# Optimization experiments

Measured on AMD Instinct MI355X. Metric: run time of the kernel, lower is better.

Reference implementation:

```python
import jax, jax.numpy as jnp
import numpy as np

EPS = 1e-8


def setup_inputs() -> dict:
    key = jax.random.key(0)
    k1, k2, k3 = jax.random.split(key, 3)
    n_nodes, n_pos, d, n_seg = 50000, 2048, 128, 32
    pred = jax.random.normal(k1, (n_nodes, d), dtype=jnp.float32)
    target = jax.random.normal(k2, (n_pos, d), dtype=jnp.float32)
    target_identifiers = jax.random.randint(k3, (n_pos,), 0, n_seg, dtype=jnp.int64)
    return {
        "pred": pred,
        "target": target,
        "target_identifiers": target_identifiers,
        "num_segments": n_seg,
    }


def reference(pred, target, target_identifiers, num_segments):
    # Pairwise L2 distance: sqrt(||t||^2 - 2 t.p + ||p||^2 + eps)
    # avoids materializing the [n_pos, n_nodes, d] broadcast tensor.
    t2 = jnp.sum(target * target, axis=-1, keepdims=True)          # [n_pos, 1]
    p2 = jnp.sum(pred * pred, axis=-1)                             # [n_nodes]
    cross = jnp.einsum('pd,nd->pn', target, pred)                  # [n_pos, n_nodes]
    sq = jnp.maximum(t2 - 2.0 * cross + p2[None, :], 0.0)
    dist_mat = jnp.sqrt(sq + EPS)                                  # [n_pos, n_nodes]

    # stage1: scatter_mean over target_identifiers (dim=0)
    seg_sum = jax.ops.segment_sum(dist_mat, target_identifiers,
                                  num_segments=num_segments)       # [n_seg, n_nodes]
    counts = jax.ops.segment_sum(jnp.ones((dist_mat.shape[0],), dist_mat.dtype),
                                 target_identifiers, num_segments=num_segments)
    seg_mean = seg_sum / jnp.maximum(counts, 1.0)[:, None]

    # stage2: mean over segments
    return seg_mean.mean(axis=0)                                   # [n_nodes]
```

## Files before the change

### kernel.cpp

```cpp
#include <hip/hip_runtime.h>

#define DIMK 128

typedef __bf16 bf16x8 __attribute__((ext_vector_type(8)));
typedef float  f32x4  __attribute__((ext_vector_type(4)));

__device__ inline unsigned short f32_to_bf16_rne(float f) {
    unsigned u = __float_as_uint(f);
    u += 0x7FFFu + ((u >> 16) & 1u);
    return (unsigned short)(u >> 16);
}


__global__ void pack_rows(const float* __restrict__ src,
                          unsigned short* __restrict__ dst,
                          float* __restrict__ norm2,
                          int n_valid, int n_rows_pad, float scale) {
    int wave = threadIdx.x >> 6, lane = threadIdx.x & 63;
    int row = blockIdx.x * 4 + wave;
    if (row >= n_rows_pad) return;
    int srow = min(row, n_valid - 1);
    int e = lane * 2;
    float2 v = *(const float2*)(src + (size_t)srow * DIMK + e);
    unsigned pk = (unsigned)f32_to_bf16_rne(scale * v.x) |
                  ((unsigned)f32_to_bf16_rne(scale * v.y) << 16);
    int tile = row >> 4, col = row & 15;
    int kk = e >> 5, kb = (e >> 3) & 3, j = e & 7;
    size_t off = (size_t)tile * 2048 + kk * 512 + (kb * 16 + col) * 8 + j;
    *(unsigned*)(dst + off) = pk;
    float s = v.x * v.x + v.y * v.y;
#pragma unroll
    for (int o = 1; o < 64; o <<= 1) s += __shfl_xor(s, o, 64);
    if (lane == 0) norm2[row] = s;
}

__global__ void seg_weights(const int* __restrict__ ids,
                            const int* __restrict__ nseg_p,
                            const float* __restrict__ t2,
                            float2* __restrict__ tw, int n_pos) {
    __shared__ int   cnt[256];
    __shared__ float w[256];
    int nseg = nseg_p[0];
    if (nseg > 256) nseg = 256;
    int t = threadIdx.x;
    if (t < nseg) cnt[t] = 0;
    __syncthreads();
    for (int p = t; p < n_pos; p += blockDim.x) atomicAdd(&cnt[ids[p]], 1);
    __syncthreads();
    if (t < nseg) w[t] = 1.0f / ((float)nseg * (float)max(cnt[t], 1));
    __syncthreads();
    for (int p = t; p < n_pos; p += blockDim.x) {
        float2 e; e.x = t2[p]; e.y = w[ids[p]];
        tw[p] = e;
    }
}

#define SLICE_TILES 8
__global__ __launch_bounds__(256, 4)
void l2dist_main(const unsigned short* __restrict__ pb,
                 const float* __restrict__ p2,
                 const unsigned short* __restrict__ tb,
                 const float2* __restrict__ tw,
                 float* __restrict__ out,
                 int n_nodes) {
    __shared__ __align__(16) unsigned short lbuf[SLICE_TILES][2048];
    __shared__ __align__(16) float tw_lds[SLICE_TILES * 32];

    const int tid  = threadIdx.x;
    const int lane = tid & 63;
    const int wave = tid >> 6;
    const int col  = lane & 15;
    const int kb   = lane >> 4;
    const int n0   = blockIdx.x * 128 + wave * 32;

    bf16x8 bfrag[2][4];
    float p2g[2];
    const unsigned short* bp = pb + ((size_t)(n0 >> 4)) * 2048 + (size_t)lane * 8;
#pragma unroll
    for (int g = 0; g < 2; ++g) {
#pragma unroll
        for (int kk = 0; kk < 4; ++kk)
            bfrag[g][kk] = *(const bf16x8*)(bp + g * 2048 + kk * 512);
        p2g[g] = p2[n0 + g * 16 + col];
    }

    const int pbase = blockIdx.y * SLICE_TILES;

    if (tid < SLICE_TILES * 16) {
        float2 e = tw[pbase * 16 + tid];
        tw_lds[2 * tid]     = e.x;
        tw_lds[2 * tid + 1] = e.y;
    }

    const unsigned short* sgp = tb + (size_t)pbase * 2048 + wave * 512 + lane * 8;
    unsigned short* ldst = &lbuf[0][0] + wave * 512;
#pragma unroll
    for (int t = 0; t < SLICE_TILES; ++t) {
        __builtin_amdgcn_global_load_lds(
            (const __attribute__((address_space(1))) unsigned int*)(const void*)
                (sgp + (size_t)t * 2048),
            (__attribute__((address_space(3))) unsigned int*)(void*)
                (ldst + t * 2048),
            16, 0, 0);
    }
    __syncthreads();

    float acc0 = 0.f, acc1 = 0.f;
#pragma unroll
    for (int t = 0; t < SLICE_TILES; ++t) {
        const unsigned short* rb = &lbuf[t][lane * 8];
        bf16x8 a0 = *(const bf16x8*)(rb);
        bf16x8 a1 = *(const bf16x8*)(rb + 512);
        bf16x8 a2 = *(const bf16x8*)(rb + 1024);
        bf16x8 a3 = *(const bf16x8*)(rb + 1536);

        f32x4 d0 = {0.f, 0.f, 0.f, 0.f};
        f32x4 d1 = {0.f, 0.f, 0.f, 0.f};
        d0 = __builtin_amdgcn_mfma_f32_16x16x32_bf16(a0, bfrag[0][0], d0, 0, 0, 0);
        d1 = __builtin_amdgcn_mfma_f32_16x16x32_bf16(a0, bfrag[1][0], d1, 0, 0, 0);
        d0 = __builtin_amdgcn_mfma_f32_16x16x32_bf16(a1, bfrag[0][1], d0, 0, 0, 0);
        d1 = __builtin_amdgcn_mfma_f32_16x16x32_bf16(a1, bfrag[1][1], d1, 0, 0, 0);
        d0 = __builtin_amdgcn_mfma_f32_16x16x32_bf16(a2, bfrag[0][2], d0, 0, 0, 0);
        d1 = __builtin_amdgcn_mfma_f32_16x16x32_bf16(a2, bfrag[1][2], d1, 0, 0, 0);
        d0 = __builtin_amdgcn_mfma_f32_16x16x32_bf16(a3, bfrag[0][3], d0, 0, 0, 0);
        d1 = __builtin_amdgcn_mfma_f32_16x16x32_bf16(a3, bfrag[1][3], d1, 0, 0, 0);

        f32x4 w0 = *(const f32x4*)&tw_lds[(t * 16 + kb * 4) * 2];
        f32x4 w1 = *(const f32x4*)&tw_lds[(t * 16 + kb * 4) * 2 + 4];
        float t2v[4] = {w0[0], w0[2], w1[0], w1[2]};
        float wv[4]  = {w0[1], w0[3], w1[1], w1[3]};
#pragma unroll
        for (int j = 0; j < 4; ++j) {
            float s0 = d0[j] + (t2v[j] + p2g[0]);
            float s1 = d1[j] + (t2v[j] + p2g[1]);
            acc0 = fmaf(wv[j], __builtin_amdgcn_sqrtf(fmaxf(s0, 0.f)), acc0);
            acc1 = fmaf(wv[j], __builtin_amdgcn_sqrtf(fmaxf(s1, 0.f)), acc1);
        }
    }

    acc0 += __shfl_xor(acc0, 16, 64);
    acc0 += __shfl_xor(acc0, 32, 64);
    acc1 += __shfl_xor(acc1, 16, 64);
    acc1 += __shfl_xor(acc1, 32, 64);
    if (lane < 16) {
        int na = n0 + col;
        int nb = n0 + 16 + col;
        if (na < n_nodes) atomicAdd(out + na, acc0);
        if (nb < n_nodes) atomicAdd(out + nb, acc1);
    }
}

extern "C" void kernel_launch(void* const* d_in, const int* in_sizes, int n_in,
                              void* d_out, int out_size, void* d_ws, size_t ws_size,
                              hipStream_t stream) {
    const float* pred  = (const float*)d_in[0];
    const float* tgt   = (const float*)d_in[1];
    const int*   ids   = (const int*)d_in[2];
    const int*   nsegp = (const int*)d_in[3];
    float* out = (float*)d_out;

    int n_nodes = in_sizes[0] / DIMK;
    int n_pos   = in_sizes[2];

    int gx = (n_nodes + 127) / 128;
    int n_rows_pad = gx * 128;

    char* ws = (char*)d_ws;
    size_t off_pb = 0;
    size_t off_tb = off_pb + (size_t)n_rows_pad * DIMK * 2;
    size_t off_p2 = off_tb + (size_t)n_pos * DIMK * 2;
    size_t off_t2 = off_p2 + (size_t)n_rows_pad * 4;
    size_t off_tw = off_t2 + (size_t)n_pos * 4;
    unsigned short* pb = (unsigned short*)(ws + off_pb);
    unsigned short* tb = (unsigned short*)(ws + off_tb);
    float*          p2 = (float*)(ws + off_p2);
    float*          t2 = (float*)(ws + off_t2);
    float2*         tw = (float2*)(ws + off_tw);

    pack_rows<<<(n_rows_pad + 3) / 4, 256, 0, stream>>>(pred, pb, p2, n_nodes, n_rows_pad, 1.0f);
    pack_rows<<<(n_pos + 3) / 4, 256, 0, stream>>>(tgt, tb, t2, n_pos, n_pos, -2.0f);
    seg_weights<<<1, 1024, 0, stream>>>(ids, nsegp, t2, tw, n_pos);
    hipMemsetAsync(out, 0, (size_t)out_size * sizeof(float), stream);

    int ys = (n_pos >> 4) / SLICE_TILES;
    dim3 grid(gx, ys);
    l2dist_main<<<grid, 256, 0, stream>>>(pb, p2, tb, tw, out, n_nodes);
}
```

Measured before the change: 58.94 us.

## Halve target slice per block, swap grid axes, prefetch weights from global

Cuts the target tiles each block processes from 8 to 4, doubling the grid and the number of atomic adds to the output. The grid axes are swapped so that consecutive blocks share the same pred rows and walk through different target slices. The per-row t2 and weight values are now read straight from global memory into registers with a one-tile-ahead prefetch, replacing the LDS staging. Launch bounds rise to 6 blocks per CU. This aims to raise occupancy and improve L2 locality for the pred fragments, at the cost of reloading pred fragments twice as often and doubling atomic traffic.

Result: slower. 62.29 us (+5.7%).

```diff
diff --git a/kernel.cpp b/kernel.cpp
--- a/kernel.cpp
+++ b/kernel.cpp
@@ -1,6 +1,7 @@
 #include <hip/hip_runtime.h>
 
 #define DIMK 128
+#define SLICE_TILES 4
 
 typedef __bf16 bf16x8 __attribute__((ext_vector_type(8)));
 typedef float  f32x4  __attribute__((ext_vector_type(4)));
@@ -55,8 +56,7 @@
     }
 }
 
-#define SLICE_TILES 8
-__global__ __launch_bounds__(256, 4)
+__global__ __launch_bounds__(256, 6)
 void l2dist_main(const unsigned short* __restrict__ pb,
                  const float* __restrict__ p2,
                  const unsigned short* __restrict__ tb,
@@ -64,14 +64,25 @@
                  float* __restrict__ out,
                  int n_nodes) {
     __shared__ __align__(16) unsigned short lbuf[SLICE_TILES][2048];
-    __shared__ __align__(16) float tw_lds[SLICE_TILES * 32];
-
     const int tid  = threadIdx.x;
     const int lane = tid & 63;
     const int wave = tid >> 6;
     const int col  = lane & 15;
     const int kb   = lane >> 4;
-    const int n0   = blockIdx.x * 128 + wave * 32;
+    const int n0   = blockIdx.y * 128 + wave * 32;
+
+    const int pbase = blockIdx.x * SLICE_TILES;
+    const unsigned short* sgp = tb + (size_t)pbase * 2048 + wave * 512 + lane * 8;
+    unsigned short* ldst = &lbuf[0][0] + wave * 512;
+#pragma unroll
+    for (int t = 0; t < SLICE_TILES; ++t) {
+        __builtin_amdgcn_global_load_lds(
+            (const __attribute__((address_space(1))) unsigned int*)(const void*)
+                (sgp + (size_t)t * 2048),
+            (__attribute__((address_space(3))) unsigned int*)(void*)
+                (ldst + t * 2048),
+            16, 0, 0);
+    }
 
     bf16x8 bfrag[2][4];
     float p2g[2];
@@ -84,30 +95,21 @@
         p2g[g] = p2[n0 + g * 16 + col];
     }
 
-    const int pbase = blockIdx.y * SLICE_TILES;
+    const float2* twp = tw + ((size_t)pbase << 4) + kb * 4;
+    f32x4 cw0 = *(const f32x4*)(twp);
+    f32x4 cw1 = *(const f32x4*)(twp + 2);
 
-    if (tid < SLICE_TILES * 16) {
-        float2 e = tw[pbase * 16 + tid];
-        tw_lds[2 * tid]     = e.x;
-        tw_lds[2 * tid + 1] = e.y;
-    }
-
-    const unsigned short* sgp = tb + (size_t)pbase * 2048 + wave * 512 + lane * 8;
-    unsigned short* ldst = &lbuf[0][0] + wave * 512;
-#pragma unroll
-    for (int t = 0; t < SLICE_TILES; ++t) {
-        __builtin_amdgcn_global_load_lds(
-            (const __attribute__((address_space(1))) unsigned int*)(const void*)
-                (sgp + (size_t)t * 2048),
-            (__attribute__((address_space(3))) unsigned int*)(void*)
-                (ldst + t * 2048),
-            16, 0, 0);
-    }
     __syncthreads();
 
     float acc0 = 0.f, acc1 = 0.f;
 #pragma unroll
     for (int t = 0; t < SLICE_TILES; ++t) {
+        f32x4 nw0 = cw0, nw1 = cw1;
+        if (t + 1 < SLICE_TILES) {
+            nw0 = *(const f32x4*)(twp + 16 * (t + 1));
+            nw1 = *(const f32x4*)(twp + 16 * (t + 1) + 2);
+        }
+
         const unsigned short* rb = &lbuf[t][lane * 8];
         bf16x8 a0 = *(const bf16x8*)(rb);
         bf16x8 a1 = *(const bf16x8*)(rb + 512);
@@ -125,10 +127,8 @@
         d0 = __builtin_amdgcn_mfma_f32_16x16x32_bf16(a3, bfrag[0][3], d0, 0, 0, 0);
         d1 = __builtin_amdgcn_mfma_f32_16x16x32_bf16(a3, bfrag[1][3], d1, 0, 0, 0);
 
-        f32x4 w0 = *(const f32x4*)&tw_lds[(t * 16 + kb * 4) * 2];
-        f32x4 w1 = *(const f32x4*)&tw_lds[(t * 16 + kb * 4) * 2 + 4];
-        float t2v[4] = {w0[0], w0[2], w1[0], w1[2]};
-        float wv[4]  = {w0[1], w0[3], w1[1], w1[3]};
+        float t2v[4] = {cw0[0], cw0[2], cw1[0], cw1[2]};
+        float wv[4]  = {cw0[1], cw0[3], cw1[1], cw1[3]};
 #pragma unroll
         for (int j = 0; j < 4; ++j) {
             float s0 = d0[j] + (t2v[j] + p2g[0]);
@@ -136,6 +136,7 @@
             acc0 = fmaf(wv[j], __builtin_amdgcn_sqrtf(fmaxf(s0, 0.f)), acc0);
             acc1 = fmaf(wv[j], __builtin_amdgcn_sqrtf(fmaxf(s1, 0.f)), acc1);
         }
+        cw0 = nw0; cw1 = nw1;
     }
 
     acc0 += __shfl_xor(acc0, 16, 64);
@@ -162,8 +163,8 @@
     int n_nodes = in_sizes[0] / DIMK;
     int n_pos   = in_sizes[2];
 
-    int gx = (n_nodes + 127) / 128;
-    int n_rows_pad = gx * 128;
+    int gy = (n_nodes + 127) / 128;
+    int n_rows_pad = gy * 128;
 
     char* ws = (char*)d_ws;
     size_t off_pb = 0;
@@ -182,7 +183,7 @@
     seg_weights<<<1, 1024, 0, stream>>>(ids, nsegp, t2, tw, n_pos);
     hipMemsetAsync(out, 0, (size_t)out_size * sizeof(float), stream);
 
-    int ys = (n_pos >> 4) / SLICE_TILES;
-    dim3 grid(gx, ys);
+    int gx = (n_pos >> 4) / SLICE_TILES;
+    dim3 grid(gx, gy);
     l2dist_main<<<grid, 256, 0, stream>>>(pb, p2, tb, tw, out, n_nodes);
 }
```

## Enlarge main-kernel tile, double-buffer target loads, fold norms into MFMA accumulator

Applied to the files above, without the earlier changes.

Each wave now covers 64 nodes instead of 32, and each block processes 256 target rows instead of 128. The target tiles are streamed through a two-slot LDS ring of async global-to-LDS loads with explicit vmcnt waits and barriers, so loads overlap with compute. t2 and p2 are preloaded into the MFMA accumulator, which removes per-element adds. The grid is reordered so the target slice is the fast dimension and node tiles are the slow one, which halves the atomics per node relative to the work done. The cost is higher register pressure from 16 B fragments and 4 accumulators, and fewer blocks for load balancing.

Result: slower. 66.82 us (+13.4%).

```diff
diff --git a/kernel.cpp b/kernel.cpp
--- a/kernel.cpp
+++ b/kernel.cpp
@@ -36,8 +36,7 @@
 
 __global__ void seg_weights(const int* __restrict__ ids,
                             const int* __restrict__ nseg_p,
-                            const float* __restrict__ t2,
-                            float2* __restrict__ tw, int n_pos) {
+                            float* __restrict__ wsa, int n_pos) {
     __shared__ int   cnt[256];
     __shared__ float w[256];
     int nseg = nseg_p[0];
@@ -49,104 +48,133 @@
     __syncthreads();
     if (t < nseg) w[t] = 1.0f / ((float)nseg * (float)max(cnt[t], 1));
     __syncthreads();
-    for (int p = t; p < n_pos; p += blockDim.x) {
-        float2 e; e.x = t2[p]; e.y = w[ids[p]];
-        tw[p] = e;
-    }
-}
-
-#define SLICE_TILES 8
+    for (int p = t; p < n_pos; p += blockDim.x) wsa[p] = w[ids[p]];
+}
+
 __global__ __launch_bounds__(256, 4)
 void l2dist_main(const unsigned short* __restrict__ pb,
                  const float* __restrict__ p2,
                  const unsigned short* __restrict__ tb,
-                 const float2* __restrict__ tw,
+                 const float* __restrict__ t2g,
+                 const float* __restrict__ wg,
                  float* __restrict__ out,
                  int n_nodes) {
-    __shared__ __align__(16) unsigned short lbuf[SLICE_TILES][2048];
-    __shared__ __align__(16) float tw_lds[SLICE_TILES * 32];
+    __shared__ __align__(16) unsigned short lbuf[2][8192];
+    __shared__ __align__(16) float t2_lds[256];
+    __shared__ __align__(16) float w_lds[256];
 
     const int tid  = threadIdx.x;
     const int lane = tid & 63;
     const int wave = tid >> 6;
     const int col  = lane & 15;
     const int kb   = lane >> 4;
-    const int n0   = blockIdx.x * 128 + wave * 32;
-
-    bf16x8 bfrag[2][4];
-    float p2g[2];
+    const int n0   = blockIdx.y * 256 + wave * 64;
+    const int tbase = blockIdx.x * 16;
+    const int rbase = tbase * 16;
+
+    bf16x8 bfrag[4][4];
+    float p2g[4];
     const unsigned short* bp = pb + ((size_t)(n0 >> 4)) * 2048 + (size_t)lane * 8;
 #pragma unroll
-    for (int g = 0; g < 2; ++g) {
+    for (int g = 0; g < 4; ++g) {
 #pragma unroll
         for (int kk = 0; kk < 4; ++kk)
             bfrag[g][kk] = *(const bf16x8*)(bp + g * 2048 + kk * 512);
         p2g[g] = p2[n0 + g * 16 + col];
     }
 
-    const int pbase = blockIdx.y * SLICE_TILES;
-
-    if (tid < SLICE_TILES * 16) {
-        float2 e = tw[pbase * 16 + tid];
-        tw_lds[2 * tid]     = e.x;
-        tw_lds[2 * tid + 1] = e.y;
-    }
-
-    const unsigned short* sgp = tb + (size_t)pbase * 2048 + wave * 512 + lane * 8;
-    unsigned short* ldst = &lbuf[0][0] + wave * 512;
-#pragma unroll
-    for (int t = 0; t < SLICE_TILES; ++t) {
-        __builtin_amdgcn_global_load_lds(
-            (const __attribute__((address_space(1))) unsigned int*)(const void*)
-                (sgp + (size_t)t * 2048),
-            (__attribute__((address_space(3))) unsigned int*)(void*)
-                (ldst + t * 2048),
-            16, 0, 0);
-    }
-    __syncthreads();
-
-    float acc0 = 0.f, acc1 = 0.f;
-#pragma unroll
-    for (int t = 0; t < SLICE_TILES; ++t) {
-        const unsigned short* rb = &lbuf[t][lane * 8];
-        bf16x8 a0 = *(const bf16x8*)(rb);
-        bf16x8 a1 = *(const bf16x8*)(rb + 512);
-        bf16x8 a2 = *(const bf16x8*)(rb + 1024);
-        bf16x8 a3 = *(const bf16x8*)(rb + 1536);
-
-        f32x4 d0 = {0.f, 0.f, 0.f, 0.f};
-        f32x4 d1 = {0.f, 0.f, 0.f, 0.f};
-        d0 = __builtin_amdgcn_mfma_f32_16x16x32_bf16(a0, bfrag[0][0], d0, 0, 0, 0);
-        d1 = __builtin_amdgcn_mfma_f32_16x16x32_bf16(a0, bfrag[1][0], d1, 0, 0, 0);
-        d0 = __builtin_amdgcn_mfma_f32_16x16x32_bf16(a1, bfrag[0][1], d0, 0, 0, 0);
-        d1 = __builtin_amdgcn_mfma_f32_16x16x32_bf16(a1, bfrag[1][1], d1, 0, 0, 0);
-        d0 = __builtin_amdgcn_mfma_f32_16x16x32_bf16(a2, bfrag[0][2], d0, 0, 0, 0);
-        d1 = __builtin_amdgcn_mfma_f32_16x16x32_bf16(a2, bfrag[1][2], d1, 0, 0, 0);
-        d0 = __builtin_amdgcn_mfma_f32_16x16x32_bf16(a3, bfrag[0][3], d0, 0, 0, 0);
-        d1 = __builtin_amdgcn_mfma_f32_16x16x32_bf16(a3, bfrag[1][3], d1, 0, 0, 0);
-
-        f32x4 w0 = *(const f32x4*)&tw_lds[(t * 16 + kb * 4) * 2];
-        f32x4 w1 = *(const f32x4*)&tw_lds[(t * 16 + kb * 4) * 2 + 4];
-        float t2v[4] = {w0[0], w0[2], w1[0], w1[2]};
-        float wv[4]  = {w0[1], w0[3], w1[1], w1[3]};
-#pragma unroll
-        for (int j = 0; j < 4; ++j) {
-            float s0 = d0[j] + (t2v[j] + p2g[0]);
-            float s1 = d1[j] + (t2v[j] + p2g[1]);
-            acc0 = fmaf(wv[j], __builtin_amdgcn_sqrtf(fmaxf(s0, 0.f)), acc0);
-            acc1 = fmaf(wv[j], __builtin_amdgcn_sqrtf(fmaxf(s1, 0.f)), acc1);
+    __builtin_amdgcn_global_load_lds(
+        (const __attribute__((address_space(1))) unsigned int*)(const void*)
+            (t2g + rbase + wave * 64 + lane),
+        (__attribute__((address_space(3))) unsigned int*)(void*)
+            (&t2_lds[wave * 64]), 4, 0, 0);
+    __builtin_amdgcn_global_load_lds(
+        (const __attribute__((address_space(1))) unsigned int*)(const void*)
+            (wg + rbase + wave * 64 + lane),
+        (__attribute__((address_space(3))) unsigned int*)(void*)
+            (&w_lds[wave * 64]), 4, 0, 0);
+
+    const unsigned short* sgp = tb + (size_t)tbase * 2048 + wave * 512 + lane * 8;
+#define STAGE(C, B)                                                            \
+    _Pragma("unroll")                                                          \
+    for (int t_ = 0; t_ < 4; ++t_) {                                           \
+        __builtin_amdgcn_global_load_lds(                                      \
+            (const __attribute__((address_space(1))) unsigned int*)(const void*)\
+                (sgp + ((C) * 4 + t_) * 2048),                                 \
+            (__attribute__((address_space(3))) unsigned int*)(void*)           \
+                (&lbuf[B][t_ * 2048] + wave * 512),                            \
+            16, 0, 0);                                                         \
+    }
+
+    STAGE(0, 0);
+    STAGE(1, 1);
+
+    float acc0 = 0.f, acc1 = 0.f, acc2 = 0.f, acc3 = 0.f;
+
+#pragma unroll
+    for (int c = 0; c < 4; ++c) {
+        if (c < 3) { asm volatile("s_waitcnt vmcnt(4)" ::: "memory"); }
+        else       { asm volatile("s_waitcnt vmcnt(0)" ::: "memory"); }
+        __builtin_amdgcn_s_barrier();
+
+#pragma unroll
+        for (int t = 0; t < 4; ++t) {
+            const unsigned short* rb = &lbuf[c & 1][t * 2048] + lane * 8;
+            bf16x8 a0 = *(const bf16x8*)(rb);
+            bf16x8 a1 = *(const bf16x8*)(rb + 512);
+            bf16x8 a2 = *(const bf16x8*)(rb + 1024);
+            bf16x8 a3 = *(const bf16x8*)(rb + 1536);
+
+            f32x4 t2v = *(const f32x4*)&t2_lds[(c * 4 + t) * 16 + kb * 4];
+            f32x4 wv  = *(const f32x4*)&w_lds[(c * 4 + t) * 16 + kb * 4];
+
+            f32x4 d0 = t2v + p2g[0];
+            f32x4 d1 = t2v + p2g[1];
+            f32x4 d2 = t2v + p2g[2];
+            f32x4 d3 = t2v + p2g[3];
+            d0 = __builtin_amdgcn_mfma_f32_16x16x32_bf16(a0, bfrag[0][0], d0, 0, 0, 0);
+            d1 = __builtin_amdgcn_mfma_f32_16x16x32_bf16(a0, bfrag[1][0], d1, 0, 0, 0);
+            d2 = __builtin_amdgcn_mfma_f32_16x16x32_bf16(a0, bfrag[2][0], d2, 0, 0, 0);
+            d3 = __builtin_amdgcn_mfma_f32_16x16x32_bf16(a0, bfrag[3][0], d3, 0, 0, 0);
+            d0 = __builtin_amdgcn_mfma_f32_16x16x32_bf16(a1, bfrag[0][1], d0, 0, 0, 0);
+            d1 = __builtin_amdgcn_mfma_f32_16x16x32_bf16(a1, bfrag[1][1], d1, 0, 0, 0);
+            d2 = __builtin_amdgcn_mfma_f32_16x16x32_bf16(a1, bfrag[2][1], d2, 0, 0, 0);
+            d3 = __builtin_amdgcn_mfma_f32_16x16x32_bf16(a1, bfrag[3][1], d3, 0, 0, 0);
+            d0 = __builtin_amdgcn_mfma_f32_16x16x32_bf16(a2, bfrag[0][2], d0, 0, 0, 0);
+            d1 = __builtin_amdgcn_mfma_f32_16x16x32_bf16(a2, bfrag[1][2], d1, 0, 0, 0);
+            d2 = __builtin_amdgcn_mfma_f32_16x16x32_bf16(a2, bfrag[2][2], d2, 0, 0, 0);
+            d3 = __builtin_amdgcn_mfma_f32_16x16x32_bf16(a2, bfrag[3][2], d3, 0, 0, 0);
+            d0 = __builtin_amdgcn_mfma_f32_16x16x32_bf16(a3, bfrag[0][3], d0, 0, 0, 0);
+            d1 = __builtin_amdgcn_mfma_f32_16x16x32_bf16(a3, bfrag[1][3], d1, 0, 0, 0);
+            d2 = __builtin_amdgcn_mfma_f32_16x16x32_bf16(a3, bfrag[2][3], d2, 0, 0, 0);
+            d3 = __builtin_amdgcn_mfma_f32_16x16x32_bf16(a3, bfrag[3][3], d3, 0, 0, 0);
+
+#pragma unroll
+            for (int j = 0; j < 4; ++j) {
+                acc0 = fmaf(wv[j], __builtin_amdgcn_sqrtf(fmaxf(d0[j], 0.f)), acc0);
+                acc1 = fmaf(wv[j], __builtin_amdgcn_sqrtf(fmaxf(d1[j], 0.f)), acc1);
+                acc2 = fmaf(wv[j], __builtin_amdgcn_sqrtf(fmaxf(d2[j], 0.f)), acc2);
+                acc3 = fmaf(wv[j], __builtin_amdgcn_sqrtf(fmaxf(d3[j], 0.f)), acc3);
+            }
         }
-    }
-
-    acc0 += __shfl_xor(acc0, 16, 64);
-    acc0 += __shfl_xor(acc0, 32, 64);
-    acc1 += __shfl_xor(acc1, 16, 64);
-    acc1 += __shfl_xor(acc1, 32, 64);
+
+        if (c < 2) {
+            __builtin_amdgcn_s_barrier();
+            STAGE(c + 2, c & 1);
+        }
+    }
+#undef STAGE
+
+    acc0 += __shfl_xor(acc0, 16, 64);  acc0 += __shfl_xor(acc0, 32, 64);
+    acc1 += __shfl_xor(acc1, 16, 64);  acc1 += __shfl_xor(acc1, 32, 64);
+    acc2 += __shfl_xor(acc2, 16, 64);  acc2 += __shfl_xor(acc2, 32, 64);
+    acc3 += __shfl_xor(acc3, 16, 64);  acc3 += __shfl_xor(acc3, 32, 64);
     if (lane < 16) {
         int na = n0 + col;
-        int nb = n0 + 16 + col;
-        if (na < n_nodes) atomicAdd(out + na, acc0);
-        if (nb < n_nodes) atomicAdd(out + nb, acc1);
+        if (na      < n_nodes) atomicAdd(out + na,      acc0);
+        if (na + 16 < n_nodes) atomicAdd(out + na + 16, acc1);
+        if (na + 32 < n_nodes) atomicAdd(out + na + 32, acc2);
+        if (na + 48 < n_nodes) atomicAdd(out + na + 48, acc3);
     }
 }
 
@@ -162,27 +190,26 @@
     int n_nodes = in_sizes[0] / DIMK;
     int n_pos   = in_sizes[2];
 
-    int gx = (n_nodes + 127) / 128;
-    int n_rows_pad = gx * 128;
+    int gy = (n_nodes + 255) / 256;
+    int n_rows_pad = gy * 256;
 
     char* ws = (char*)d_ws;
     size_t off_pb = 0;
     size_t off_tb = off_pb + (size_t)n_rows_pad * DIMK * 2;
     size_t off_p2 = off_tb + (size_t)n_pos * DIMK * 2;
     size_t off_t2 = off_p2 + (size_t)n_rows_pad * 4;
-    size_t off_tw = off_t2 + (size_t)n_pos * 4;
-    unsigned short* pb = (unsigned short*)(ws + off_pb);
-    unsigned short* tb = (unsigned short*)(ws + off_tb);
-    float*          p2 = (float*)(ws + off_p2);
-    float*          t2 = (float*)(ws + off_t2);
-    float2*         tw = (float2*)(ws + off_tw);
+    size_t off_w  = off_t2 + (size_t)n_pos * 4;
+    unsigned short* pb  = (unsigned short*)(ws + off_pb);
+    unsigned short* tb  = (unsigned short*)(ws + off_tb);
+    float*          p2  = (float*)(ws + off_p2);
+    float*          t2  = (float*)(ws + off_t2);
+    float*          wsa = (float*)(ws + off_w);
 
     pack_rows<<<(n_rows_pad + 3) / 4, 256, 0, stream>>>(pred, pb, p2, n_nodes, n_rows_pad, 1.0f);
     pack_rows<<<(n_pos + 3) / 4, 256, 0, stream>>>(tgt, tb, t2, n_pos, n_pos, -2.0f);
-    seg_weights<<<1, 1024, 0, stream>>>(ids, nsegp, t2, tw, n_pos);
+    seg_weights<<<1, 1024, 0, stream>>>(ids, nsegp, wsa, n_pos);
     hipMemsetAsync(out, 0, (size_t)out_size * sizeof(float), stream);
 
-    int ys = (n_pos >> 4) / SLICE_TILES;
-    dim3 grid(gx, ys);
-    l2dist_main<<<grid, 256, 0, stream>>>(pb, p2, tb, tw, out, n_nodes);
-}
+    dim3 grid(n_pos / 256, gy);
+    l2dist_main<<<grid, 256, 0, stream>>>(pb, p2, tb, t2, wsa, out, n_nodes);
+}
```

## Swap grid axes, split MFMA chains, stagger LDS tiles, seed accumulators with norms

Applied to the files above, without the earlier changes.

The grid is transposed so blockIdx.x walks the target-position slices and blockIdx.y walks node blocks. Adjacent blocks now share the same pred tiles, which should improve L2 locality for the large packed pred array. Each tile's four dependent MFMAs are split into two independent accumulator chains to shorten the dependency latency, and the first chain is seeded with t2+p2 so the adds are folded in. Waves start on different LDS tiles to reduce bank conflicts, and t2 and the weights move into separate arrays so each can be read with one vector load. The target LDS load is issued before the pred fragment loads to overlap them.

New measurement: 56.07 us. 1.05x faster.

```diff
diff --git a/kernel.cpp b/kernel.cpp
--- a/kernel.cpp
+++ b/kernel.cpp
@@ -1,6 +1,8 @@
 #include <hip/hip_runtime.h>
 
 #define DIMK 128
+#define SLICE_TILES 8
+#define NODES_PER_BLOCK 128
 
 typedef __bf16 bf16x8 __attribute__((ext_vector_type(8)));
 typedef float  f32x4  __attribute__((ext_vector_type(4)));
@@ -36,8 +38,7 @@
 
 __global__ void seg_weights(const int* __restrict__ ids,
                             const int* __restrict__ nseg_p,
-                            const float* __restrict__ t2,
-                            float2* __restrict__ tw, int n_pos) {
+                            float* __restrict__ wsa, int n_pos) {
     __shared__ int   cnt[256];
     __shared__ float w[256];
     int nseg = nseg_p[0];
@@ -49,29 +50,45 @@
     __syncthreads();
     if (t < nseg) w[t] = 1.0f / ((float)nseg * (float)max(cnt[t], 1));
     __syncthreads();
-    for (int p = t; p < n_pos; p += blockDim.x) {
-        float2 e; e.x = t2[p]; e.y = w[ids[p]];
-        tw[p] = e;
-    }
+    for (int p = t; p < n_pos; p += blockDim.x) wsa[p] = w[ids[p]];
 }
 
-#define SLICE_TILES 8
 __global__ __launch_bounds__(256, 4)
 void l2dist_main(const unsigned short* __restrict__ pb,
                  const float* __restrict__ p2,
                  const unsigned short* __restrict__ tb,
-                 const float2* __restrict__ tw,
+                 const float* __restrict__ t2g,
+                 const float* __restrict__ wg,
                  float* __restrict__ out,
                  int n_nodes) {
     __shared__ __align__(16) unsigned short lbuf[SLICE_TILES][2048];
-    __shared__ __align__(16) float tw_lds[SLICE_TILES * 32];
+    __shared__ __align__(16) float t2_lds[SLICE_TILES * 16];
+    __shared__ __align__(16) float w_lds[SLICE_TILES * 16];
 
     const int tid  = threadIdx.x;
     const int lane = tid & 63;
     const int wave = tid >> 6;
     const int col  = lane & 15;
     const int kb   = lane >> 4;
-    const int n0   = blockIdx.x * 128 + wave * 32;
+    const int n0   = blockIdx.y * NODES_PER_BLOCK + wave * 32;
+
+    const int pbase = blockIdx.x * SLICE_TILES;
+    const unsigned short* sgp = tb + (size_t)pbase * 2048 + wave * 512 + lane * 8;
+    unsigned short* ldst = &lbuf[0][0] + wave * 512;
+#pragma unroll
+    for (int t = 0; t < SLICE_TILES; ++t) {
+        __builtin_amdgcn_global_load_lds(
+            (const __attribute__((address_space(1))) unsigned int*)(const void*)
+                (sgp + (size_t)t * 2048),
+            (__attribute__((address_space(3))) unsigned int*)(void*)
+                (ldst + t * 2048),
+            16, 0, 0);
+    }
+
+    if (tid < SLICE_TILES * 16) {
+        t2_lds[tid] = t2g[pbase * 16 + tid];
+        w_lds[tid]  = wg[pbase * 16 + tid];
+    }
 
     bf16x8 bfrag[2][4];
     float p2g[2];
@@ -84,57 +101,41 @@
         p2g[g] = p2[n0 + g * 16 + col];
     }
 
-    const int pbase = blockIdx.y * SLICE_TILES;
-
-    if (tid < SLICE_TILES * 16) {
-        float2 e = tw[pbase * 16 + tid];
-        tw_lds[2 * tid]     = e.x;
-        tw_lds[2 * tid + 1] = e.y;
-    }
-
-    const unsigned short* sgp = tb + (size_t)pbase * 2048 + wave * 512 + lane * 8;
-    unsigned short* ldst = &lbuf[0][0] + wave * 512;
-#pragma unroll
-    for (int t = 0; t < SLICE_TILES; ++t) {
-        __builtin_amdgcn_global_load_lds(
-            (const __attribute__((address_space(1))) unsigned int*)(const void*)
-                (sgp + (size_t)t * 2048),
-            (__attribute__((address_space(3))) unsigned int*)(void*)
-                (ldst + t * 2048),
-            16, 0, 0);
-    }
     __syncthreads();
 
     float acc0 = 0.f, acc1 = 0.f;
 #pragma unroll
     for (int t = 0; t < SLICE_TILES; ++t) {
-        const unsigned short* rb = &lbuf[t][lane * 8];
+        const int te = (t + 2 * wave) & (SLICE_TILES - 1);
+
+        const unsigned short* rb = &lbuf[te][lane * 8];
         bf16x8 a0 = *(const bf16x8*)(rb);
         bf16x8 a1 = *(const bf16x8*)(rb + 512);
         bf16x8 a2 = *(const bf16x8*)(rb + 1024);
         bf16x8 a3 = *(const bf16x8*)(rb + 1536);
 
-        f32x4 d0 = {0.f, 0.f, 0.f, 0.f};
-        f32x4 d1 = {0.f, 0.f, 0.f, 0.f};
-        d0 = __builtin_amdgcn_mfma_f32_16x16x32_bf16(a0, bfrag[0][0], d0, 0, 0, 0);
-        d1 = __builtin_amdgcn_mfma_f32_16x16x32_bf16(a0, bfrag[1][0], d1, 0, 0, 0);
-        d0 = __builtin_amdgcn_mfma_f32_16x16x32_bf16(a1, bfrag[0][1], d0, 0, 0, 0);
-        d1 = __builtin_amdgcn_mfma_f32_16x16x32_bf16(a1, bfrag[1][1], d1, 0, 0, 0);
-        d0 = __builtin_amdgcn_mfma_f32_16x16x32_bf16(a2, bfrag[0][2], d0, 0, 0, 0);
-        d1 = __builtin_amdgcn_mfma_f32_16x16x32_bf16(a2, bfrag[1][2], d1, 0, 0, 0);
-        d0 = __builtin_amdgcn_mfma_f32_16x16x32_bf16(a3, bfrag[0][3], d0, 0, 0, 0);
-        d1 = __builtin_amdgcn_mfma_f32_16x16x32_bf16(a3, bfrag[1][3], d1, 0, 0, 0);
+        f32x4 t2v = *(const f32x4*)&t2_lds[te * 16 + kb * 4];
+        f32x4 wv  = *(const f32x4*)&w_lds[te * 16 + kb * 4];
 
-        f32x4 w0 = *(const f32x4*)&tw_lds[(t * 16 + kb * 4) * 2];
-        f32x4 w1 = *(const f32x4*)&tw_lds[(t * 16 + kb * 4) * 2 + 4];
-        float t2v[4] = {w0[0], w0[2], w1[0], w1[2]};
-        float wv[4]  = {w0[1], w0[3], w1[1], w1[3]};
+        f32x4 d0a = t2v + p2g[0];
+        f32x4 d1a = t2v + p2g[1];
+        f32x4 d0b = {0.f, 0.f, 0.f, 0.f};
+        f32x4 d1b = {0.f, 0.f, 0.f, 0.f};
+        d0a = __builtin_amdgcn_mfma_f32_16x16x32_bf16(a0, bfrag[0][0], d0a, 0, 0, 0);
+        d1a = __builtin_amdgcn_mfma_f32_16x16x32_bf16(a0, bfrag[1][0], d1a, 0, 0, 0);
+        d0b = __builtin_amdgcn_mfma_f32_16x16x32_bf16(a2, bfrag[0][2], d0b, 0, 0, 0);
+        d1b = __builtin_amdgcn_mfma_f32_16x16x32_bf16(a2, bfrag[1][2], d1b, 0, 0, 0);
+        d0a = __builtin_amdgcn_mfma_f32_16x16x32_bf16(a1, bfrag[0][1], d0a, 0, 0, 0);
+        d1a = __builtin_amdgcn_mfma_f32_16x16x32_bf16(a1, bfrag[1][1], d1a, 0, 0, 0);
+        d0b = __builtin_amdgcn_mfma_f32_16x16x32_bf16(a3, bfrag[0][3], d0b, 0, 0, 0);
+        d1b = __builtin_amdgcn_mfma_f32_16x16x32_bf16(a3, bfrag[1][3], d1b, 0, 0, 0);
+
+        f32x4 s0 = d0a + d0b;
+        f32x4 s1 = d1a + d1b;
 #pragma unroll
         for (int j = 0; j < 4; ++j) {
-            float s0 = d0[j] + (t2v[j] + p2g[0]);
-            float s1 = d1[j] + (t2v[j] + p2g[1]);
-            acc0 = fmaf(wv[j], __builtin_amdgcn_sqrtf(fmaxf(s0, 0.f)), acc0);
-            acc1 = fmaf(wv[j], __builtin_amdgcn_sqrtf(fmaxf(s1, 0.f)), acc1);
+            acc0 = fmaf(wv[j], __builtin_amdgcn_sqrtf(fmaxf(s0[j], 0.f)), acc0);
+            acc1 = fmaf(wv[j], __builtin_amdgcn_sqrtf(fmaxf(s1[j], 0.f)), acc1);
         }
     }
 
@@ -144,9 +145,8 @@
     acc1 += __shfl_xor(acc1, 32, 64);
     if (lane < 16) {
         int na = n0 + col;
-        int nb = n0 + 16 + col;
-        if (na < n_nodes) atomicAdd(out + na, acc0);
-        if (nb < n_nodes) atomicAdd(out + nb, acc1);
+        if (na      < n_nodes) atomicAdd(out + na,      acc0);
+        if (na + 16 < n_nodes) atomicAdd(out + na + 16, acc1);
     }
 }
 
@@ -162,27 +162,27 @@
     int n_nodes = in_sizes[0] / DIMK;
     int n_pos   = in_sizes[2];
 
-    int gx = (n_nodes + 127) / 128;
-    int n_rows_pad = gx * 128;
+    int gy = (n_nodes + NODES_PER_BLOCK - 1) / NODES_PER_BLOCK;
+    int n_rows_pad = gy * NODES_PER_BLOCK;
 
     char* ws = (char*)d_ws;
     size_t off_pb = 0;
     size_t off_tb = off_pb + (size_t)n_rows_pad * DIMK * 2;
     size_t off_p2 = off_tb + (size_t)n_pos * DIMK * 2;
     size_t off_t2 = off_p2 + (size_t)n_rows_pad * 4;
-    size_t off_tw = off_t2 + (size_t)n_pos * 4;
-    unsigned short* pb = (unsigned short*)(ws + off_pb);
-    unsigned short* tb = (unsigned short*)(ws + off_tb);
-    float*          p2 = (float*)(ws + off_p2);
-    float*          t2 = (float*)(ws + off_t2);
-    float2*         tw = (float2*)(ws + off_tw);
+    size_t off_w  = off_t2 + (size_t)n_pos * 4;
+    unsigned short* pb  = (unsigned short*)(ws + off_pb);
+    unsigned short* tb  = (unsigned short*)(ws + off_tb);
+    float*          p2  = (float*)(ws + off_p2);
+    float*          t2  = (float*)(ws + off_t2);
+    float*          wsa = (float*)(ws + off_w);
 
     pack_rows<<<(n_rows_pad + 3) / 4, 256, 0, stream>>>(pred, pb, p2, n_nodes, n_rows_pad, 1.0f);
     pack_rows<<<(n_pos + 3) / 4, 256, 0, stream>>>(tgt, tb, t2, n_pos, n_pos, -2.0f);
-    seg_weights<<<1, 1024, 0, stream>>>(ids, nsegp, t2, tw, n_pos);
+    seg_weights<<<1, 1024, 0, stream>>>(ids, nsegp, wsa, n_pos);
     hipMemsetAsync(out, 0, (size_t)out_size * sizeof(float), stream);
 
-    int ys = (n_pos >> 4) / SLICE_TILES;
-    dim3 grid(gx, ys);
-    l2dist_main<<<grid, 256, 0, stream>>>(pb, p2, tb, tw, out, n_nodes);
+    int gx = (n_pos >> 4) / SLICE_TILES;
+    dim3 grid(gx, gy);
+    l2dist_main<<<grid, 256, 0, stream>>>(pb, p2, tb, t2, wsa, out, n_nodes);
 }
```
